# Performance work log

Measured on AMD Instinct MI355X. Metric: run time of the kernel, lower is better.

The kernel has to match this reference:

```python
import jax, jax.numpy as jnp
import numpy as np

N, L, C, K = 8, 16384, 256, 64  # batch, points, d_color, anchor_num; d_struct = 4*K = 256


def setup_inputs() -> dict:
    key = jax.random.key(0)
    ks = jax.random.split(key, 12)
    d_in = C + 4 * K  # 512
    s1, s2, s3 = 1.0 / np.sqrt(d_in), 1.0 / np.sqrt(128), 1.0 / np.sqrt(256)
    return {
        'feat0': jax.random.normal(ks[0], (N, L, C), jnp.float32),
        'feat1': jax.random.normal(ks[1], (N, L, C), jnp.float32),
        'pts_3d0': jax.random.normal(ks[2], (N, L, 3), jnp.float32),
        'pts_3d1': jax.random.normal(ks[3], (N, L, 3), jnp.float32),
        'anchor_i': jax.random.randint(ks[4], (N, K), 0, L, jnp.int32),
        'anchor_j': jax.random.randint(ks[5], (N, K), 0, L, jnp.int32),
        'W1': jax.random.uniform(ks[6], (d_in, 128), jnp.float32, -s1, s1),
        'b1': jax.random.uniform(ks[7], (128,), jnp.float32, -s1, s1),
        'W2': jax.random.uniform(ks[8], (128, 256), jnp.float32, -s2, s2),
        'b2': jax.random.uniform(ks[9], (256,), jnp.float32, -s2, s2),
        'W3': jax.random.uniform(ks[10], (256, C), jnp.float32, -s3, s3),
        'b3': jax.random.uniform(ks[11], (C,), jnp.float32, -s3, s3),
    }


def _structured(pts, anchor_idx):
    # pts: [N,L,3], anchor_idx: [N,K] -> [N,L,4K]
    anchors = jnp.take_along_axis(pts, anchor_idx[:, :, None], axis=1)  # [N,K,3]
    diff = pts[:, :, None, :] - anchors[:, None, :, :]                  # [N,L,K,3]
    dist = jnp.sum(diff * diff, axis=-1, keepdims=True)                 # [N,L,K,1]
    f = jnp.concatenate([diff, dist], axis=-1)                          # [N,L,K,4]
    f = f / jnp.sum(jnp.abs(f), axis=-2, keepdims=True)                 # L1 norm over K
    f = jnp.swapaxes(f, -1, -2).reshape(pts.shape[0], pts.shape[1], -1)  # [N,L,4K]
    # original l1_norm is @torch.no_grad -> structured feature is detached
    return jax.lax.stop_gradient(f)


def _mlp(x, W1, b1, W2, b2, W3, b3):
    h = jax.nn.relu(x @ W1 + b1)
    h = jax.nn.relu(h @ W2 + b2)  # dropout is identity in eval
    return h @ W3 + b3


def reference(feat0, feat1, pts_3d0, pts_3d1, anchor_i, anchor_j,
              W1, b1, W2, b2, W3, b3):
    s0 = _structured(pts_3d0, anchor_i)
    s1 = _structured(pts_3d1, anchor_j)
    aug0 = _mlp(jnp.concatenate([feat0, s0], axis=-1), W1, b1, W2, b2, W3, b3)
    aug1 = _mlp(jnp.concatenate([feat1, s1], axis=-1), W1, b1, W2, b2, W3, b3)
    return aug0, aug1
```

## Files before the change

kernel.cpp:

```cpp
#include <hip/hip_runtime.h>

typedef __bf16 bf16x8 __attribute__((ext_vector_type(8)));
typedef float f32x4 __attribute__((ext_vector_type(4)));
typedef unsigned short u16x4 __attribute__((ext_vector_type(4)));
typedef unsigned short u16x8 __attribute__((ext_vector_type(8)));

#define NBATCH 8
#define LPTS   16384
#define CDIM   256
#define KANC   64
#define DIN    512
#define H1DIM  128
#define H2DIM  256
#define TM     64

__device__ __forceinline__ unsigned short f2b(float f){
  __bf16 h = (__bf16)f;
  return __builtin_bit_cast(unsigned short, h);
}

__global__ __launch_bounds__(256) void prep_weights(
    const float* __restrict__ W1, const float* __restrict__ W2,
    const float* __restrict__ W3, unsigned short* __restrict__ wt){
  int id = blockIdx.x * 256 + threadIdx.x;
  if (id < 65536){
    int r = id >> 9, c = id & 511;
    wt[id] = f2b(W1[c * 128 + r]);
  } else if (id < 98304){
    int t = id - 65536; int r = t >> 7, c = t & 127;
    wt[id] = f2b(W2[c * 256 + r]);
  } else if (id < 163840){
    int t = id - 98304; int r = t >> 8, c = t & 255;
    wt[id] = f2b(W3[c * 256 + r]);
  }
}

__global__ __launch_bounds__(512, 4) void fused(
    const float* __restrict__ feat0, const float* __restrict__ feat1,
    const float* __restrict__ pts0, const float* __restrict__ pts1,
    const int* __restrict__ anc_i, const int* __restrict__ anc_j,
    const float* __restrict__ b1, const float* __restrict__ b2,
    const float* __restrict__ b3, const unsigned short* __restrict__ wt,
    float* __restrict__ out)
{
  __shared__ unsigned short xs[TM * DIN];
  __shared__ unsigned short h1s[TM * H1DIM];
  unsigned short* h2s = xs;
  float4* anc4 = (float4*)h1s;

  const int tid  = threadIdx.x;
  const int wg   = blockIdx.x;
  const int strm = wg >> 11;
  const int n    = (wg >> 8) & 7;
  const int l0   = (wg & 255) * TM;

  const float* feat = strm ? feat1 : feat0;
  const float* pts  = strm ? pts1 : pts0;
  const int*   anci = strm ? anc_j : anc_i;

  const float* pp = pts + ((size_t)n * LPTS + l0 + (tid >> 3)) * 3;
  float px = pp[0], py = pp[1], pz = pp[2];

  if (tid < KANC){
    int ai = anci[n * KANC + tid];
    const float* ap = pts + ((size_t)n * LPTS + ai) * 3;
    anc4[tid + (tid >> 3)] = make_float4(ap[0], ap[1], ap[2], 0.f);
  }

  {
    const float4* fb = (const float4*)(feat + ((size_t)n * LPTS + l0) * CDIM);
    #pragma unroll
    for (int it = 0; it < 8; ++it){
      int flat = it * 512 + tid;
      int r = flat >> 6, c4 = flat & 63;
      float4 v = fb[flat];
      int e = (r * DIN + c4 * 4) ^ ((r & 7) << 3);
      u16x4 pk = { f2b(v.x), f2b(v.y), f2b(v.z), f2b(v.w) };
      *(u16x4*)&xs[e] = pk;
    }
  }
  __syncthreads();

  {
    const int l   = tid >> 3;
    const int sub = tid & 7;
    float s0 = 0.f, s1 = 0.f, s2 = 0.f, s3 = 0.f;
    #pragma unroll
    for (int i = 0; i < 8; ++i){
      float4 a = anc4[sub * 9 + i];
      float dx = px - a.x, dy = py - a.y, dz = pz - a.z;
      float d2 = dx*dx + dy*dy + dz*dz;
      s0 += fabsf(dx); s1 += fabsf(dy); s2 += fabsf(dz); s3 += d2;
    }
    #pragma unroll
    for (int m = 1; m <= 4; m <<= 1){
      s0 += __shfl_xor(s0, m, 64);
      s1 += __shfl_xor(s1, m, 64);
      s2 += __shfl_xor(s2, m, 64);
      s3 += __shfl_xor(s3, m, 64);
    }
    float i0 = 1.f/s0, i1 = 1.f/s1, i2 = 1.f/s2, i3 = 1.f/s3;

    u16x8 o0, o1, o2, o3;
    #pragma unroll
    for (int i = 0; i < 8; ++i){
      float4 a = anc4[sub * 9 + i];
      float dx = px - a.x, dy = py - a.y, dz = pz - a.z;
      float d2 = dx*dx + dy*dy + dz*dz;
      o0[i] = f2b(dx * i0); o1[i] = f2b(dy * i1);
      o2[i] = f2b(dz * i2); o3[i] = f2b(d2 * i3);
    }
    int base = l * DIN + 256 + sub * 8;
    int swl = (l & 7) << 3;
    *(u16x8*)&xs[(base      ) ^ swl] = o0;
    *(u16x8*)&xs[(base +  64) ^ swl] = o1;
    *(u16x8*)&xs[(base + 128) ^ swl] = o2;
    *(u16x8*)&xs[(base + 192) ^ swl] = o3;
  }
  __syncthreads();

  const int lane = tid & 63;
  const int w    = tid >> 6;
  const int lr   = lane & 15;
  const int lg   = lane >> 4;

  {
    f32x4 acc[4] = {};
    const int col = w * 16 + lr;
    const unsigned short* wrow = wt + col * DIN;
    #pragma unroll 4
    for (int kk = 0; kk < 16; ++kk){
      int kb = kk * 32 + lg * 8;
      bf16x8 b = *(const bf16x8*)&wrow[kb];
      #pragma unroll
      for (int m = 0; m < 4; ++m){
        int row = m * 16 + lr;
        int e = (row * DIN + kb) ^ ((row & 7) << 3);
        bf16x8 a = *(const bf16x8*)&xs[e];
        acc[m] = __builtin_amdgcn_mfma_f32_16x16x32_bf16(a, b, acc[m], 0, 0, 0);
      }
    }
    float bias = b1[col];
    #pragma unroll
    for (int m = 0; m < 4; ++m){
      #pragma unroll
      for (int r = 0; r < 4; ++r){
        int row = m * 16 + lg * 4 + r;
        float v = fmaxf(acc[m][r] + bias, 0.f);
        int e = (row * H1DIM + col) ^ ((row & 7) << 3);
        h1s[e] = f2b(v);
      }
    }
  }
  __syncthreads();

  {
    const unsigned short* w2t = wt + 65536;
    f32x4 acc[4][2] = {};
    const int col0 = w * 32;
    #pragma unroll
    for (int kk = 0; kk < 4; ++kk){
      int kb = kk * 32 + lg * 8;
      bf16x8 bf0 = *(const bf16x8*)&w2t[(col0 + lr) * H1DIM + kb];
      bf16x8 bf1 = *(const bf16x8*)&w2t[(col0 + 16 + lr) * H1DIM + kb];
      #pragma unroll
      for (int m = 0; m < 4; ++m){
        int row = m * 16 + lr;
        int e = (row * H1DIM + kb) ^ ((row & 7) << 3);
        bf16x8 a = *(const bf16x8*)&h1s[e];
        acc[m][0] = __builtin_amdgcn_mfma_f32_16x16x32_bf16(a, bf0, acc[m][0], 0, 0, 0);
        acc[m][1] = __builtin_amdgcn_mfma_f32_16x16x32_bf16(a, bf1, acc[m][1], 0, 0, 0);
      }
    }
    __syncthreads();
    #pragma unroll
    for (int nt = 0; nt < 2; ++nt){
      int col = col0 + nt * 16 + lr;
      float bias = b2[col];
      #pragma unroll
      for (int m = 0; m < 4; ++m){
        #pragma unroll
        for (int r = 0; r < 4; ++r){
          int row = m * 16 + lg * 4 + r;
          float v = fmaxf(acc[m][nt][r] + bias, 0.f);
          int e = (row * H2DIM + col) ^ ((row & 7) << 3);
          h2s[e] = f2b(v);
        }
      }
    }
  }
  __syncthreads();

  {
    const unsigned short* w3t = wt + 98304;
    f32x4 acc[4][2] = {};
    const int col0 = w * 32;
    #pragma unroll 4
    for (int kk = 0; kk < 8; ++kk){
      int kb = kk * 32 + lg * 8;
      bf16x8 bf0 = *(const bf16x8*)&w3t[(col0 + lr) * H2DIM + kb];
      bf16x8 bf1 = *(const bf16x8*)&w3t[(col0 + 16 + lr) * H2DIM + kb];
      #pragma unroll
      for (int m = 0; m < 4; ++m){
        int row = m * 16 + lr;
        int e = (row * H2DIM + kb) ^ ((row & 7) << 3);
        bf16x8 a = *(const bf16x8*)&h2s[e];
        acc[m][0] = __builtin_amdgcn_mfma_f32_16x16x32_bf16(a, bf0, acc[m][0], 0, 0, 0);
        acc[m][1] = __builtin_amdgcn_mfma_f32_16x16x32_bf16(a, bf1, acc[m][1], 0, 0, 0);
      }
    }
    float* ob = out + (((size_t)strm * NBATCH + n) * LPTS + l0) * CDIM;
    #pragma unroll
    for (int nt = 0; nt < 2; ++nt){
      int col = col0 + nt * 16 + lr;
      float bias = b3[col];
      #pragma unroll
      for (int m = 0; m < 4; ++m){
        #pragma unroll
        for (int r = 0; r < 4; ++r){
          int row = m * 16 + lg * 4 + r;
          ob[(size_t)row * CDIM + col] = acc[m][nt][r] + bias;
        }
      }
    }
  }
}

extern "C" void kernel_launch(void* const* d_in, const int* in_sizes, int n_in,
                              void* d_out, int out_size, void* d_ws, size_t ws_size,
                              hipStream_t stream){
  const float* feat0 = (const float*)d_in[0];
  const float* feat1 = (const float*)d_in[1];
  const float* pts0  = (const float*)d_in[2];
  const float* pts1  = (const float*)d_in[3];
  const int*   anci  = (const int*)d_in[4];
  const int*   ancj  = (const int*)d_in[5];
  const float* W1    = (const float*)d_in[6];
  const float* b1    = (const float*)d_in[7];
  const float* W2    = (const float*)d_in[8];
  const float* b2    = (const float*)d_in[9];
  const float* W3    = (const float*)d_in[10];
  const float* b3    = (const float*)d_in[11];
  unsigned short* wt = (unsigned short*)d_ws;
  float* out = (float*)d_out;

  prep_weights<<<640, 256, 0, stream>>>(W1, W2, W3, wt);
  fused<<<4096, 512, 0, stream>>>(feat0, feat1, pts0, pts1, anci, ancj,
                                  b1, b2, b3, wt, out);
}
```

Measured before the change: 226.9 us.

## Make fused MLP kernel persistent over 8 tiles with register-prefetched inputs

Each workgroup now handles 8 consecutive 64-row tiles instead of one, cutting the grid from 4096 to 512 blocks. The feature and point loads for the next tile are issued into registers while the current tile's structured features and GEMMs run, overlapping global reads with compute. Bias values are hoisted out of the loop, and barriers become a custom lgkmcnt-wait plus s_barrier that does not wait on outstanding global loads. The costs are higher register pressure from the prefetch buffer, fewer blocks to fill the GPU (512 for 256 CUs), and the anchor table being reloaded into shared memory every iteration.

```diff
diff --git a/kernel.cpp b/kernel.cpp
--- a/kernel.cpp
+++ b/kernel.cpp
@@ -18,6 +18,12 @@
   __bf16 h = (__bf16)f;
   return __builtin_bit_cast(unsigned short, h);
 }
+
+#define LBAR() do{ \
+  asm volatile("s_waitcnt lgkmcnt(0)" ::: "memory"); \
+  __builtin_amdgcn_s_barrier(); \
+  asm volatile("" ::: "memory"); \
+} while(0)
 
 __global__ __launch_bounds__(256) void prep_weights(
     const float* __restrict__ W1, const float* __restrict__ W2,
@@ -49,180 +55,202 @@
   float4* anc4 = (float4*)h1s;
 
   const int tid  = threadIdx.x;
-  const int wg   = blockIdx.x;
-  const int strm = wg >> 11;
-  const int n    = (wg >> 8) & 7;
-  const int l0   = (wg & 255) * TM;
+  const int b    = blockIdx.x;
+  const int strm = b >> 8;
+  const int n    = (b >> 5) & 7;
+  const int tb   = b & 31;
 
   const float* feat = strm ? feat1 : feat0;
   const float* pts  = strm ? pts1 : pts0;
   const int*   anci = strm ? anc_j : anc_i;
 
-  const float* pp = pts + ((size_t)n * LPTS + l0 + (tid >> 3)) * 3;
-  float px = pp[0], py = pp[1], pz = pp[2];
+  const int lane = tid & 63;
+  const int w    = tid >> 6;
+  const int lr   = lane & 15, lg = lane >> 4;
+
+  const int col1 = w * 16 + lr;
+  const unsigned short* wrow1 = wt + col1 * DIN;
+  const float bias1v = b1[col1];
+  const int col23 = w * 32;
+  const float bias2v0 = b2[col23 + lr], bias2v1 = b2[col23 + 16 + lr];
+  const float bias3v0 = b3[col23 + lr], bias3v1 = b3[col23 + 16 + lr];
+  const unsigned short* w2t = wt + 65536;
+  const unsigned short* w3t = wt + 98304;
+
+  const size_t fB = (size_t)n * LPTS;
 
   if (tid < KANC){
     int ai = anci[n * KANC + tid];
-    const float* ap = pts + ((size_t)n * LPTS + ai) * 3;
+    const float* ap = pts + (fB + ai) * 3;
     anc4[tid + (tid >> 3)] = make_float4(ap[0], ap[1], ap[2], 0.f);
   }
 
+  float4 fv[8];
   {
-    const float4* fb = (const float4*)(feat + ((size_t)n * LPTS + l0) * CDIM);
+    const float4* fb = (const float4*)(feat + (fB + tb * 512) * CDIM);
+    #pragma unroll
+    for (int it = 0; it < 8; ++it) fv[it] = fb[it * 512 + tid];
+  }
+  float px, py, pz;
+  {
+    const float* pp = pts + (fB + tb * 512 + (tid >> 3)) * 3;
+    px = pp[0]; py = pp[1]; pz = pp[2];
+  }
+  __syncthreads();
+
+  #pragma unroll 1
+  for (int i = 0; i < 8; ++i){
+    const int l0i = tb * 512 + i * 64;
+
     #pragma unroll
     for (int it = 0; it < 8; ++it){
       int flat = it * 512 + tid;
       int r = flat >> 6, c4 = flat & 63;
-      float4 v = fb[flat];
+      float4 v = fv[it];
       int e = (r * DIN + c4 * 4) ^ ((r & 7) << 3);
       u16x4 pk = { f2b(v.x), f2b(v.y), f2b(v.z), f2b(v.w) };
       *(u16x4*)&xs[e] = pk;
     }
-  }
-  __syncthreads();
-
-  {
-    const int l   = tid >> 3;
-    const int sub = tid & 7;
-    float s0 = 0.f, s1 = 0.f, s2 = 0.f, s3 = 0.f;
-    #pragma unroll
-    for (int i = 0; i < 8; ++i){
-      float4 a = anc4[sub * 9 + i];
-      float dx = px - a.x, dy = py - a.y, dz = pz - a.z;
-      float d2 = dx*dx + dy*dy + dz*dz;
-      s0 += fabsf(dx); s1 += fabsf(dy); s2 += fabsf(dz); s3 += d2;
-    }
-    #pragma unroll
-    for (int m = 1; m <= 4; m <<= 1){
-      s0 += __shfl_xor(s0, m, 64);
-      s1 += __shfl_xor(s1, m, 64);
-      s2 += __shfl_xor(s2, m, 64);
-      s3 += __shfl_xor(s3, m, 64);
-    }
-    float i0 = 1.f/s0, i1 = 1.f/s1, i2 = 1.f/s2, i3 = 1.f/s3;
-
-    u16x8 o0, o1, o2, o3;
-    #pragma unroll
-    for (int i = 0; i < 8; ++i){
-      float4 a = anc4[sub * 9 + i];
-      float dx = px - a.x, dy = py - a.y, dz = pz - a.z;
-      float d2 = dx*dx + dy*dy + dz*dz;
-      o0[i] = f2b(dx * i0); o1[i] = f2b(dy * i1);
-      o2[i] = f2b(dz * i2); o3[i] = f2b(d2 * i3);
-    }
-    int base = l * DIN + 256 + sub * 8;
-    int swl = (l & 7) << 3;
-    *(u16x8*)&xs[(base      ) ^ swl] = o0;
-    *(u16x8*)&xs[(base +  64) ^ swl] = o1;
-    *(u16x8*)&xs[(base + 128) ^ swl] = o2;
-    *(u16x8*)&xs[(base + 192) ^ swl] = o3;
-  }
-  __syncthreads();
-
-  const int lane = tid & 63;
-  const int w    = tid >> 6;
-  const int lr   = lane & 15;
-  const int lg   = lane >> 4;
-
-  {
-    f32x4 acc[4] = {};
-    const int col = w * 16 + lr;
-    const unsigned short* wrow = wt + col * DIN;
-    #pragma unroll 4
-    for (int kk = 0; kk < 16; ++kk){
-      int kb = kk * 32 + lg * 8;
-      bf16x8 b = *(const bf16x8*)&wrow[kb];
-      #pragma unroll
-      for (int m = 0; m < 4; ++m){
-        int row = m * 16 + lr;
-        int e = (row * DIN + kb) ^ ((row & 7) << 3);
-        bf16x8 a = *(const bf16x8*)&xs[e];
-        acc[m] = __builtin_amdgcn_mfma_f32_16x16x32_bf16(a, b, acc[m], 0, 0, 0);
-      }
-    }
-    float bias = b1[col];
-    #pragma unroll
-    for (int m = 0; m < 4; ++m){
-      #pragma unroll
-      for (int r = 0; r < 4; ++r){
-        int row = m * 16 + lg * 4 + r;
-        float v = fmaxf(acc[m][r] + bias, 0.f);
-        int e = (row * H1DIM + col) ^ ((row & 7) << 3);
-        h1s[e] = f2b(v);
-      }
-    }
-  }
-  __syncthreads();
-
-  {
-    const unsigned short* w2t = wt + 65536;
-    f32x4 acc[4][2] = {};
-    const int col0 = w * 32;
-    #pragma unroll
-    for (int kk = 0; kk < 4; ++kk){
-      int kb = kk * 32 + lg * 8;
-      bf16x8 bf0 = *(const bf16x8*)&w2t[(col0 + lr) * H1DIM + kb];
-      bf16x8 bf1 = *(const bf16x8*)&w2t[(col0 + 16 + lr) * H1DIM + kb];
-      #pragma unroll
-      for (int m = 0; m < 4; ++m){
-        int row = m * 16 + lr;
-        int e = (row * H1DIM + kb) ^ ((row & 7) << 3);
-        bf16x8 a = *(const bf16x8*)&h1s[e];
-        acc[m][0] = __builtin_amdgcn_mfma_f32_16x16x32_bf16(a, bf0, acc[m][0], 0, 0, 0);
-        acc[m][1] = __builtin_amdgcn_mfma_f32_16x16x32_bf16(a, bf1, acc[m][1], 0, 0, 0);
-      }
-    }
-    __syncthreads();
-    #pragma unroll
-    for (int nt = 0; nt < 2; ++nt){
-      int col = col0 + nt * 16 + lr;
-      float bias = b2[col];
+
+    {
+      const int l = tid >> 3, sub = tid & 7;
+      float s0 = 0.f, s1 = 0.f, s2 = 0.f, s3 = 0.f;
+      #pragma unroll
+      for (int k = 0; k < 8; ++k){
+        float4 a = anc4[sub * 9 + k];
+        float dx = px - a.x, dy = py - a.y, dz = pz - a.z;
+        float d2 = dx*dx + dy*dy + dz*dz;
+        s0 += fabsf(dx); s1 += fabsf(dy); s2 += fabsf(dz); s3 += d2;
+      }
+      #pragma unroll
+      for (int m = 1; m <= 4; m <<= 1){
+        s0 += __shfl_xor(s0, m, 64);
+        s1 += __shfl_xor(s1, m, 64);
+        s2 += __shfl_xor(s2, m, 64);
+        s3 += __shfl_xor(s3, m, 64);
+      }
+      float i0 = 1.f/s0, i1 = 1.f/s1, i2 = 1.f/s2, i3 = 1.f/s3;
+
+      u16x8 o0, o1, o2, o3;
+      #pragma unroll
+      for (int k = 0; k < 8; ++k){
+        float4 a = anc4[sub * 9 + k];
+        float dx = px - a.x, dy = py - a.y, dz = pz - a.z;
+        float d2 = dx*dx + dy*dy + dz*dz;
+        o0[k] = f2b(dx * i0); o1[k] = f2b(dy * i1);
+        o2[k] = f2b(dz * i2); o3[k] = f2b(d2 * i3);
+      }
+      int base = l * DIN + 256 + sub * 8;
+      int swl = (l & 7) << 3;
+      *(u16x8*)&xs[(base      ) ^ swl] = o0;
+      *(u16x8*)&xs[(base +  64) ^ swl] = o1;
+      *(u16x8*)&xs[(base + 128) ^ swl] = o2;
+      *(u16x8*)&xs[(base + 192) ^ swl] = o3;
+    }
+
+    if (i < 7){
+      const float4* fbn = (const float4*)(feat + (fB + l0i + 64) * CDIM);
+      #pragma unroll
+      for (int it = 0; it < 8; ++it) fv[it] = fbn[it * 512 + tid];
+      const float* ppn = pts + (fB + l0i + 64 + (tid >> 3)) * 3;
+      px = ppn[0]; py = ppn[1]; pz = ppn[2];
+    }
+    LBAR();
+
+    {
+      f32x4 acc[4] = {};
+      #pragma unroll 4
+      for (int kk = 0; kk < 16; ++kk){
+        int kb = kk * 32 + lg * 8;
+        bf16x8 bfr = *(const bf16x8*)&wrow1[kb];
+        #pragma unroll
+        for (int m = 0; m < 4; ++m){
+          int row = m * 16 + lr;
+          bf16x8 a = *(const bf16x8*)&xs[(row * DIN + kb) ^ ((row & 7) << 3)];
+          acc[m] = __builtin_amdgcn_mfma_f32_16x16x32_bf16(a, bfr, acc[m], 0, 0, 0);
+        }
+      }
       #pragma unroll
       for (int m = 0; m < 4; ++m){
         #pragma unroll
         for (int r = 0; r < 4; ++r){
           int row = m * 16 + lg * 4 + r;
-          float v = fmaxf(acc[m][nt][r] + bias, 0.f);
-          int e = (row * H2DIM + col) ^ ((row & 7) << 3);
-          h2s[e] = f2b(v);
-        }
-      }
-    }
-  }
-  __syncthreads();
-
-  {
-    const unsigned short* w3t = wt + 98304;
-    f32x4 acc[4][2] = {};
-    const int col0 = w * 32;
-    #pragma unroll 4
-    for (int kk = 0; kk < 8; ++kk){
-      int kb = kk * 32 + lg * 8;
-      bf16x8 bf0 = *(const bf16x8*)&w3t[(col0 + lr) * H2DIM + kb];
-      bf16x8 bf1 = *(const bf16x8*)&w3t[(col0 + 16 + lr) * H2DIM + kb];
-      #pragma unroll
-      for (int m = 0; m < 4; ++m){
-        int row = m * 16 + lr;
-        int e = (row * H2DIM + kb) ^ ((row & 7) << 3);
-        bf16x8 a = *(const bf16x8*)&h2s[e];
-        acc[m][0] = __builtin_amdgcn_mfma_f32_16x16x32_bf16(a, bf0, acc[m][0], 0, 0, 0);
-        acc[m][1] = __builtin_amdgcn_mfma_f32_16x16x32_bf16(a, bf1, acc[m][1], 0, 0, 0);
-      }
-    }
-    float* ob = out + (((size_t)strm * NBATCH + n) * LPTS + l0) * CDIM;
-    #pragma unroll
-    for (int nt = 0; nt < 2; ++nt){
-      int col = col0 + nt * 16 + lr;
-      float bias = b3[col];
-      #pragma unroll
-      for (int m = 0; m < 4; ++m){
-        #pragma unroll
-        for (int r = 0; r < 4; ++r){
-          int row = m * 16 + lg * 4 + r;
-          ob[(size_t)row * CDIM + col] = acc[m][nt][r] + bias;
-        }
-      }
-    }
+          float v = fmaxf(acc[m][r] + bias1v, 0.f);
+          h1s[(row * H1DIM + col1) ^ ((row & 7) << 3)] = f2b(v);
+        }
+      }
+    }
+    LBAR();
+
+    {
+      f32x4 acc[4][2] = {};
+      #pragma unroll
+      for (int kk = 0; kk < 4; ++kk){
+        int kb = kk * 32 + lg * 8;
+        bf16x8 bf0 = *(const bf16x8*)&w2t[(col23 + lr) * H1DIM + kb];
+        bf16x8 bf1 = *(const bf16x8*)&w2t[(col23 + 16 + lr) * H1DIM + kb];
+        #pragma unroll
+        for (int m = 0; m < 4; ++m){
+          int row = m * 16 + lr;
+          bf16x8 a = *(const bf16x8*)&h1s[(row * H1DIM + kb) ^ ((row & 7) << 3)];
+          acc[m][0] = __builtin_amdgcn_mfma_f32_16x16x32_bf16(a, bf0, acc[m][0], 0, 0, 0);
+          acc[m][1] = __builtin_amdgcn_mfma_f32_16x16x32_bf16(a, bf1, acc[m][1], 0, 0, 0);
+        }
+      }
+      LBAR();
+      #pragma unroll
+      for (int nt = 0; nt < 2; ++nt){
+        float bias = nt ? bias2v1 : bias2v0;
+        int col = col23 + nt * 16 + lr;
+        #pragma unroll
+        for (int m = 0; m < 4; ++m){
+          #pragma unroll
+          for (int r = 0; r < 4; ++r){
+            int row = m * 16 + lg * 4 + r;
+            float v = fmaxf(acc[m][nt][r] + bias, 0.f);
+            h2s[(row * H2DIM + col) ^ ((row & 7) << 3)] = f2b(v);
+          }
+        }
+      }
+    }
+    LBAR();
+
+    {
+      if (i < 7 && tid < KANC){
+        int ai = anci[n * KANC + tid];
+        const float* ap = pts + (fB + ai) * 3;
+        anc4[tid + (tid >> 3)] = make_float4(ap[0], ap[1], ap[2], 0.f);
+      }
+      f32x4 acc[4][2] = {};
+      #pragma unroll 4
+      for (int kk = 0; kk < 8; ++kk){
+        int kb = kk * 32 + lg * 8;
+        bf16x8 bf0 = *(const bf16x8*)&w3t[(col23 + lr) * H2DIM + kb];
+        bf16x8 bf1 = *(const bf16x8*)&w3t[(col23 + 16 + lr) * H2DIM + kb];
+        #pragma unroll
+        for (int m = 0; m < 4; ++m){
+          int row = m * 16 + lr;
+          bf16x8 a = *(const bf16x8*)&h2s[(row * H2DIM + kb) ^ ((row & 7) << 3)];
+          acc[m][0] = __builtin_amdgcn_mfma_f32_16x16x32_bf16(a, bf0, acc[m][0], 0, 0, 0);
+          acc[m][1] = __builtin_amdgcn_mfma_f32_16x16x32_bf16(a, bf1, acc[m][1], 0, 0, 0);
+        }
+      }
+      float* ob = out + (((size_t)strm * NBATCH + n) * LPTS + l0i) * CDIM;
+      #pragma unroll
+      for (int nt = 0; nt < 2; ++nt){
+        float bias = nt ? bias3v1 : bias3v0;
+        int col = col23 + nt * 16 + lr;
+        #pragma unroll
+        for (int m = 0; m < 4; ++m){
+          #pragma unroll
+          for (int r = 0; r < 4; ++r){
+            int row = m * 16 + lg * 4 + r;
+            ob[(size_t)row * CDIM + col] = acc[m][nt][r] + bias;
+          }
+        }
+      }
+    }
+    LBAR();
   }
 }
 
@@ -245,6 +273,6 @@
   float* out = (float*)d_out;
 
   prep_weights<<<640, 256, 0, stream>>>(W1, W2, W3, wt);
-  fused<<<4096, 512, 0, stream>>>(feat0, feat1, pts0, pts1, anci, ancj,
-                                  b1, b2, b3, wt, out);
-}
+  fused<<<512, 512, 0, stream>>>(feat0, feat1, pts0, pts1, anci, ancj,
+                                 b1, b2, b3, wt, out);
+}
```

Result: slower. 517.4 us (+128.0%).

## Stream feat directly into layer-1 MFMA operands and shrink LDS tile

Applied to the files above, without the earlier changes.

Layer 1 no longer stages the color features in shared memory. Each wave now loads fp32 feat rows from global memory, converts them to bf16 in registers and feeds them straight to MFMA, while LDS holds only the structured half of the input. Layer 1 is re-tiled into a 2x4 wave grid with 32x32 output blocks. The smaller LDS footprint lets the launch bounds ask for 6 blocks per CU instead of 4, and a barrier in layer 2 that is now redundant is removed. The cost is that the four column-waves sharing a row block each re-read the same feat rows, relying on cache hits, and global load latency now sits directly in the MFMA loop.

```diff
diff --git a/kernel.cpp b/kernel.cpp
--- a/kernel.cpp
+++ b/kernel.cpp
@@ -2,7 +2,6 @@
 
 typedef __bf16 bf16x8 __attribute__((ext_vector_type(8)));
 typedef float f32x4 __attribute__((ext_vector_type(4)));
-typedef unsigned short u16x4 __attribute__((ext_vector_type(4)));
 typedef unsigned short u16x8 __attribute__((ext_vector_type(8)));
 
 #define NBATCH 8
@@ -17,6 +16,13 @@
 __device__ __forceinline__ unsigned short f2b(float f){
   __bf16 h = (__bf16)f;
   return __builtin_bit_cast(unsigned short, h);
+}
+
+__device__ __forceinline__ bf16x8 cvt8(float4 a, float4 b){
+  bf16x8 r;
+  r[0]=(__bf16)a.x; r[1]=(__bf16)a.y; r[2]=(__bf16)a.z; r[3]=(__bf16)a.w;
+  r[4]=(__bf16)b.x; r[5]=(__bf16)b.y; r[6]=(__bf16)b.z; r[7]=(__bf16)b.w;
+  return r;
 }
 
 __global__ __launch_bounds__(256) void prep_weights(
@@ -35,7 +41,7 @@
   }
 }
 
-__global__ __launch_bounds__(512, 4) void fused(
+__global__ __launch_bounds__(512, 6) void fused(
     const float* __restrict__ feat0, const float* __restrict__ feat1,
     const float* __restrict__ pts0, const float* __restrict__ pts1,
     const int* __restrict__ anc_i, const int* __restrict__ anc_j,
@@ -43,7 +49,7 @@
     const float* __restrict__ b3, const unsigned short* __restrict__ wt,
     float* __restrict__ out)
 {
-  __shared__ unsigned short xs[TM * DIN];
+  __shared__ unsigned short xs[TM * 256];
   __shared__ unsigned short h1s[TM * H1DIM];
   unsigned short* h2s = xs;
   float4* anc4 = (float4*)h1s;
@@ -58,26 +64,15 @@
   const float* pts  = strm ? pts1 : pts0;
   const int*   anci = strm ? anc_j : anc_i;
 
-  const float* pp = pts + ((size_t)n * LPTS + l0 + (tid >> 3)) * 3;
+  const size_t fB = (size_t)n * LPTS;
+
+  const float* pp = pts + (fB + l0 + (tid >> 3)) * 3;
   float px = pp[0], py = pp[1], pz = pp[2];
 
   if (tid < KANC){
     int ai = anci[n * KANC + tid];
-    const float* ap = pts + ((size_t)n * LPTS + ai) * 3;
+    const float* ap = pts + (fB + ai) * 3;
     anc4[tid + (tid >> 3)] = make_float4(ap[0], ap[1], ap[2], 0.f);
-  }
-
-  {
-    const float4* fb = (const float4*)(feat + ((size_t)n * LPTS + l0) * CDIM);
-    #pragma unroll
-    for (int it = 0; it < 8; ++it){
-      int flat = it * 512 + tid;
-      int r = flat >> 6, c4 = flat & 63;
-      float4 v = fb[flat];
-      int e = (r * DIN + c4 * 4) ^ ((r & 7) << 3);
-      u16x4 pk = { f2b(v.x), f2b(v.y), f2b(v.z), f2b(v.w) };
-      *(u16x4*)&xs[e] = pk;
-    }
   }
   __syncthreads();
 
@@ -110,7 +105,7 @@
       o0[i] = f2b(dx * i0); o1[i] = f2b(dy * i1);
       o2[i] = f2b(dz * i2); o3[i] = f2b(d2 * i3);
     }
-    int base = l * DIN + 256 + sub * 8;
+    int base = l * 256 + sub * 8;
     int swl = (l & 7) << 3;
     *(u16x8*)&xs[(base      ) ^ swl] = o0;
     *(u16x8*)&xs[(base +  64) ^ swl] = o1;
@@ -121,34 +116,54 @@
 
   const int lane = tid & 63;
   const int w    = tid >> 6;
-  const int lr   = lane & 15;
-  const int lg   = lane >> 4;
-
-  {
-    f32x4 acc[4] = {};
-    const int col = w * 16 + lr;
-    const unsigned short* wrow = wt + col * DIN;
-    #pragma unroll 4
-    for (int kk = 0; kk < 16; ++kk){
-      int kb = kk * 32 + lg * 8;
-      bf16x8 b = *(const bf16x8*)&wrow[kb];
-      #pragma unroll
-      for (int m = 0; m < 4; ++m){
-        int row = m * 16 + lr;
-        int e = (row * DIN + kb) ^ ((row & 7) << 3);
-        bf16x8 a = *(const bf16x8*)&xs[e];
-        acc[m] = __builtin_amdgcn_mfma_f32_16x16x32_bf16(a, b, acc[m], 0, 0, 0);
-      }
-    }
-    float bias = b1[col];
-    #pragma unroll
-    for (int m = 0; m < 4; ++m){
-      #pragma unroll
-      for (int r = 0; r < 4; ++r){
-        int row = m * 16 + lg * 4 + r;
-        float v = fmaxf(acc[m][r] + bias, 0.f);
-        int e = (row * H1DIM + col) ^ ((row & 7) << 3);
-        h1s[e] = f2b(v);
+  const int lr   = lane & 15, lg = lane >> 4;
+
+  {
+    const int wr = w >> 2, wc = w & 3;
+    f32x4 acc[2][2] = {};
+    const float* f0 = feat + (fB + l0 + wr * 32 + lr) * (size_t)CDIM;
+    const float* f1 = f0 + 16 * (size_t)CDIM;
+    const unsigned short* bq0 = wt + (wc * 32      + lr) * DIN;
+    const unsigned short* bq1 = wt + (wc * 32 + 16 + lr) * DIN;
+
+    #pragma unroll
+    for (int kk = 0; kk < 8; ++kk){
+      int kf = kk * 32 + lg * 8;
+      bf16x8 b0  = *(const bf16x8*)&bq0[kf];
+      bf16x8 b1v = *(const bf16x8*)&bq1[kf];
+      float4 lo0 = *(const float4*)&f0[kf], hi0 = *(const float4*)&f0[kf + 4];
+      float4 lo1 = *(const float4*)&f1[kf], hi1 = *(const float4*)&f1[kf + 4];
+      bf16x8 a0 = cvt8(lo0, hi0), a1 = cvt8(lo1, hi1);
+      acc[0][0] = __builtin_amdgcn_mfma_f32_16x16x32_bf16(a0, b0,  acc[0][0], 0, 0, 0);
+      acc[0][1] = __builtin_amdgcn_mfma_f32_16x16x32_bf16(a0, b1v, acc[0][1], 0, 0, 0);
+      acc[1][0] = __builtin_amdgcn_mfma_f32_16x16x32_bf16(a1, b0,  acc[1][0], 0, 0, 0);
+      acc[1][1] = __builtin_amdgcn_mfma_f32_16x16x32_bf16(a1, b1v, acc[1][1], 0, 0, 0);
+    }
+    const int row0 = wr * 32 + lr, row1 = row0 + 16;
+    #pragma unroll
+    for (int kk = 0; kk < 8; ++kk){
+      int ks = kk * 32 + lg * 8;
+      bf16x8 b0  = *(const bf16x8*)&bq0[256 + ks];
+      bf16x8 b1v = *(const bf16x8*)&bq1[256 + ks];
+      bf16x8 a0 = *(const bf16x8*)&xs[(row0 * 256 + ks) ^ ((row0 & 7) << 3)];
+      bf16x8 a1 = *(const bf16x8*)&xs[(row1 * 256 + ks) ^ ((row1 & 7) << 3)];
+      acc[0][0] = __builtin_amdgcn_mfma_f32_16x16x32_bf16(a0, b0,  acc[0][0], 0, 0, 0);
+      acc[0][1] = __builtin_amdgcn_mfma_f32_16x16x32_bf16(a0, b1v, acc[0][1], 0, 0, 0);
+      acc[1][0] = __builtin_amdgcn_mfma_f32_16x16x32_bf16(a1, b0,  acc[1][0], 0, 0, 0);
+      acc[1][1] = __builtin_amdgcn_mfma_f32_16x16x32_bf16(a1, b1v, acc[1][1], 0, 0, 0);
+    }
+    #pragma unroll
+    for (int nn = 0; nn < 2; ++nn){
+      int col = wc * 32 + nn * 16 + lr;
+      float bias = b1[col];
+      #pragma unroll
+      for (int m = 0; m < 2; ++m){
+        #pragma unroll
+        for (int r = 0; r < 4; ++r){
+          int row = wr * 32 + m * 16 + lg * 4 + r;
+          float v = fmaxf(acc[m][nn][r] + bias, 0.f);
+          h1s[(row * H1DIM + col) ^ ((row & 7) << 3)] = f2b(v);
+        }
       }
     }
   }
@@ -166,13 +181,11 @@
       #pragma unroll
       for (int m = 0; m < 4; ++m){
         int row = m * 16 + lr;
-        int e = (row * H1DIM + kb) ^ ((row & 7) << 3);
-        bf16x8 a = *(const bf16x8*)&h1s[e];
+        bf16x8 a = *(const bf16x8*)&h1s[(row * H1DIM + kb) ^ ((row & 7) << 3)];
         acc[m][0] = __builtin_amdgcn_mfma_f32_16x16x32_bf16(a, bf0, acc[m][0], 0, 0, 0);
         acc[m][1] = __builtin_amdgcn_mfma_f32_16x16x32_bf16(a, bf1, acc[m][1], 0, 0, 0);
       }
     }
-    __syncthreads();
     #pragma unroll
     for (int nt = 0; nt < 2; ++nt){
       int col = col0 + nt * 16 + lr;
@@ -183,8 +196,7 @@
         for (int r = 0; r < 4; ++r){
           int row = m * 16 + lg * 4 + r;
           float v = fmaxf(acc[m][nt][r] + bias, 0.f);
-          int e = (row * H2DIM + col) ^ ((row & 7) << 3);
-          h2s[e] = f2b(v);
+          h2s[(row * H2DIM + col) ^ ((row & 7) << 3)] = f2b(v);
         }
       }
     }
@@ -203,8 +215,7 @@
       #pragma unroll
       for (int m = 0; m < 4; ++m){
         int row = m * 16 + lr;
-        int e = (row * H2DIM + kb) ^ ((row & 7) << 3);
-        bf16x8 a = *(const bf16x8*)&h2s[e];
+        bf16x8 a = *(const bf16x8*)&h2s[(row * H2DIM + kb) ^ ((row & 7) << 3)];
         acc[m][0] = __builtin_amdgcn_mfma_f32_16x16x32_bf16(a, bf0, acc[m][0], 0, 0, 0);
         acc[m][1] = __builtin_amdgcn_mfma_f32_16x16x32_bf16(a, bf1, acc[m][1], 0, 0, 0);
       }
```

New measurement: 379.7 us. 67.3% more time.

## Fold structured-feature GEMM into per-batch coefficients, halving layer-1 K dimension

Applied to the files above, without the earlier changes.

The structured anchor features are linear in a few per-point scalars (p, |p|^2 and the L1 normalisers), so their contribution to layer 1 is rewritten as 11 per-column coefficients precomputed per (stream, batch) in a small prep kernel. The fused kernel now stages only the 256 colour channels in LDS, runs half the layer-1 MFMA iterations, and adds the structured term in the epilogue from per-row scalars. Less LDS also allows a higher occupancy hint, and one barrier in layer 2 is removed. The structured term is now computed in fp32 rather than through bf16 inputs, which changes rounding, and the squared-distance sum is expanded algebraically, which risks cancellation.

```diff
diff --git a/kernel.cpp b/kernel.cpp
--- a/kernel.cpp
+++ b/kernel.cpp
@@ -3,7 +3,6 @@
 typedef __bf16 bf16x8 __attribute__((ext_vector_type(8)));
 typedef float f32x4 __attribute__((ext_vector_type(4)));
 typedef unsigned short u16x4 __attribute__((ext_vector_type(4)));
-typedef unsigned short u16x8 __attribute__((ext_vector_type(8)));
 
 #define NBATCH 8
 #define LPTS   16384
@@ -35,16 +34,59 @@
   }
 }
 
-__global__ __launch_bounds__(512, 4) void fused(
+__global__ __launch_bounds__(128) void prep_coef(
+    const float* __restrict__ pts0, const float* __restrict__ pts1,
+    const int* __restrict__ anc_i, const int* __restrict__ anc_j,
+    const float* __restrict__ W1, float* __restrict__ coef){
+  const int comb = blockIdx.x;
+  const int strm = comb >> 3, n = comb & 7;
+  const int col  = threadIdx.x;
+  __shared__ float4 anc[64];
+  const float* pts  = strm ? pts1 : pts0;
+  const int*   anci = strm ? anc_j : anc_i;
+  if (col < 64){
+    int ai = anci[n * KANC + col];
+    const float* ap = pts + ((size_t)n * LPTS + ai) * 3;
+    anc[col] = make_float4(ap[0], ap[1], ap[2], 0.f);
+  }
+  __syncthreads();
+  float SX=0,CX=0,SY=0,CY=0,SZ=0,CZ=0,SD=0,ADx=0,ADy=0,ADz=0,CD2=0;
+  float SAx=0,SAy=0,SAz=0,SA2=0;
+  for (int k = 0; k < KANC; ++k){
+    float4 a = anc[k];
+    float ak2 = a.x*a.x + a.y*a.y + a.z*a.z;
+    float wx = W1[(256 + k) * 128 + col];
+    float wy = W1[(320 + k) * 128 + col];
+    float wz = W1[(384 + k) * 128 + col];
+    float wd = W1[(448 + k) * 128 + col];
+    SX += wx; CX += a.x * wx;
+    SY += wy; CY += a.y * wy;
+    SZ += wz; CZ += a.z * wz;
+    SD += wd; ADx += a.x * wd; ADy += a.y * wd; ADz += a.z * wd;
+    CD2 += ak2 * wd;
+    SAx += a.x; SAy += a.y; SAz += a.z; SA2 += ak2;
+  }
+  float* cf = coef + (size_t)comb * 12 * 128;
+  cf[ 0*128+col]=SX;  cf[ 1*128+col]=CX;  cf[ 2*128+col]=SY;  cf[ 3*128+col]=CY;
+  cf[ 4*128+col]=SZ;  cf[ 5*128+col]=CZ;  cf[ 6*128+col]=SD;  cf[ 7*128+col]=ADx;
+  cf[ 8*128+col]=ADy; cf[ 9*128+col]=ADz; cf[10*128+col]=CD2;
+  if (col == 0) cf[11*128+0] = SAx;
+  if (col == 1) cf[11*128+1] = SAy;
+  if (col == 2) cf[11*128+2] = SAz;
+  if (col == 3) cf[11*128+3] = SA2;
+}
+
+__global__ __launch_bounds__(512, 6) void fused(
     const float* __restrict__ feat0, const float* __restrict__ feat1,
     const float* __restrict__ pts0, const float* __restrict__ pts1,
     const int* __restrict__ anc_i, const int* __restrict__ anc_j,
     const float* __restrict__ b1, const float* __restrict__ b2,
     const float* __restrict__ b3, const unsigned short* __restrict__ wt,
-    float* __restrict__ out)
+    const float* __restrict__ coef, float* __restrict__ out)
 {
-  __shared__ unsigned short xs[TM * DIN];
+  __shared__ unsigned short xs[TM * 256];
   __shared__ unsigned short h1s[TM * H1DIM];
+  __shared__ float scal[TM][12];
   unsigned short* h2s = xs;
   float4* anc4 = (float4*)h1s;
 
@@ -57,9 +99,11 @@
   const float* feat = strm ? feat1 : feat0;
   const float* pts  = strm ? pts1 : pts0;
   const int*   anci = strm ? anc_j : anc_i;
+  const float* cf   = coef + (size_t)((strm << 3) | n) * 12 * 128;
 
   const float* pp = pts + ((size_t)n * LPTS + l0 + (tid >> 3)) * 3;
   float px = pp[0], py = pp[1], pz = pp[2];
+  float SAx = cf[11*128+0], SAy = cf[11*128+1], SAz = cf[11*128+2], SA2 = cf[11*128+3];
 
   if (tid < KANC){
     int ai = anci[n * KANC + tid];
@@ -74,7 +118,7 @@
       int flat = it * 512 + tid;
       int r = flat >> 6, c4 = flat & 63;
       float4 v = fb[flat];
-      int e = (r * DIN + c4 * 4) ^ ((r & 7) << 3);
+      int e = (r * 256 + c4 * 4) ^ ((r & 7) << 3);
       u16x4 pk = { f2b(v.x), f2b(v.y), f2b(v.z), f2b(v.w) };
       *(u16x4*)&xs[e] = pk;
     }
@@ -84,38 +128,37 @@
   {
     const int l   = tid >> 3;
     const int sub = tid & 7;
-    float s0 = 0.f, s1 = 0.f, s2 = 0.f, s3 = 0.f;
+    float s0 = 0.f, s1 = 0.f, s2 = 0.f;
     #pragma unroll
     for (int i = 0; i < 8; ++i){
       float4 a = anc4[sub * 9 + i];
-      float dx = px - a.x, dy = py - a.y, dz = pz - a.z;
-      float d2 = dx*dx + dy*dy + dz*dz;
-      s0 += fabsf(dx); s1 += fabsf(dy); s2 += fabsf(dz); s3 += d2;
+      s0 += fabsf(px - a.x); s1 += fabsf(py - a.y); s2 += fabsf(pz - a.z);
     }
     #pragma unroll
     for (int m = 1; m <= 4; m <<= 1){
       s0 += __shfl_xor(s0, m, 64);
       s1 += __shfl_xor(s1, m, 64);
       s2 += __shfl_xor(s2, m, 64);
-      s3 += __shfl_xor(s3, m, 64);
-    }
+    }
+    float pp2 = px*px + py*py + pz*pz;
+    float s3 = 64.f * pp2 - 2.f * (px*SAx + py*SAy + pz*SAz) + SA2;
     float i0 = 1.f/s0, i1 = 1.f/s1, i2 = 1.f/s2, i3 = 1.f/s3;
-
-    u16x8 o0, o1, o2, o3;
-    #pragma unroll
-    for (int i = 0; i < 8; ++i){
-      float4 a = anc4[sub * 9 + i];
-      float dx = px - a.x, dy = py - a.y, dz = pz - a.z;
-      float d2 = dx*dx + dy*dy + dz*dz;
-      o0[i] = f2b(dx * i0); o1[i] = f2b(dy * i1);
-      o2[i] = f2b(dz * i2); o3[i] = f2b(d2 * i3);
-    }
-    int base = l * DIN + 256 + sub * 8;
-    int swl = (l & 7) << 3;
-    *(u16x8*)&xs[(base      ) ^ swl] = o0;
-    *(u16x8*)&xs[(base +  64) ^ swl] = o1;
-    *(u16x8*)&xs[(base + 128) ^ swl] = o2;
-    *(u16x8*)&xs[(base + 192) ^ swl] = o3;
+    float u;
+    switch (sub){
+      case 0: u = i0 * px;       break;
+      case 1: u = -i0;           break;
+      case 2: u = i1 * py;       break;
+      case 3: u = -i1;           break;
+      case 4: u = i2 * pz;       break;
+      case 5: u = -i2;           break;
+      case 6: u = i3 * pp2;      break;
+      default: u = -2.f*i3*px;   break;
+    }
+    scal[l][sub] = u;
+    if (sub < 3){
+      float u2 = (sub == 0) ? -2.f*i3*py : (sub == 1) ? -2.f*i3*pz : i3;
+      scal[l][8 + sub] = u2;
+    }
   }
   __syncthreads();
 
@@ -128,15 +171,17 @@
     f32x4 acc[4] = {};
     const int col = w * 16 + lr;
     const unsigned short* wrow = wt + col * DIN;
+    float cc[11];
+    #pragma unroll
+    for (int j = 0; j < 11; ++j) cc[j] = cf[j * 128 + col];
     #pragma unroll 4
-    for (int kk = 0; kk < 16; ++kk){
+    for (int kk = 0; kk < 8; ++kk){
       int kb = kk * 32 + lg * 8;
       bf16x8 b = *(const bf16x8*)&wrow[kb];
       #pragma unroll
       for (int m = 0; m < 4; ++m){
         int row = m * 16 + lr;
-        int e = (row * DIN + kb) ^ ((row & 7) << 3);
-        bf16x8 a = *(const bf16x8*)&xs[e];
+        bf16x8 a = *(const bf16x8*)&xs[(row * 256 + kb) ^ ((row & 7) << 3)];
         acc[m] = __builtin_amdgcn_mfma_f32_16x16x32_bf16(a, b, acc[m], 0, 0, 0);
       }
     }
@@ -146,9 +191,15 @@
       #pragma unroll
       for (int r = 0; r < 4; ++r){
         int row = m * 16 + lg * 4 + r;
-        float v = fmaxf(acc[m][r] + bias, 0.f);
-        int e = (row * H1DIM + col) ^ ((row & 7) << 3);
-        h1s[e] = f2b(v);
+        f32x4 ua = *(const f32x4*)&scal[row][0];
+        f32x4 ub = *(const f32x4*)&scal[row][4];
+        f32x4 uc = *(const f32x4*)&scal[row][8];
+        float s = acc[m][r] + bias;
+        s += ua[0]*cc[0] + ua[1]*cc[1] + ua[2]*cc[2] + ua[3]*cc[3];
+        s += ub[0]*cc[4] + ub[1]*cc[5] + ub[2]*cc[6] + ub[3]*cc[7];
+        s += uc[0]*cc[8] + uc[1]*cc[9] + uc[2]*cc[10];
+        float v = fmaxf(s, 0.f);
+        h1s[(row * H1DIM + col) ^ ((row & 7) << 3)] = f2b(v);
       }
     }
   }
@@ -166,13 +217,11 @@
       #pragma unroll
       for (int m = 0; m < 4; ++m){
         int row = m * 16 + lr;
-        int e = (row * H1DIM + kb) ^ ((row & 7) << 3);
-        bf16x8 a = *(const bf16x8*)&h1s[e];
+        bf16x8 a = *(const bf16x8*)&h1s[(row * H1DIM + kb) ^ ((row & 7) << 3)];
         acc[m][0] = __builtin_amdgcn_mfma_f32_16x16x32_bf16(a, bf0, acc[m][0], 0, 0, 0);
         acc[m][1] = __builtin_amdgcn_mfma_f32_16x16x32_bf16(a, bf1, acc[m][1], 0, 0, 0);
       }
     }
-    __syncthreads();
     #pragma unroll
     for (int nt = 0; nt < 2; ++nt){
       int col = col0 + nt * 16 + lr;
@@ -183,8 +232,7 @@
         for (int r = 0; r < 4; ++r){
           int row = m * 16 + lg * 4 + r;
           float v = fmaxf(acc[m][nt][r] + bias, 0.f);
-          int e = (row * H2DIM + col) ^ ((row & 7) << 3);
-          h2s[e] = f2b(v);
+          h2s[(row * H2DIM + col) ^ ((row & 7) << 3)] = f2b(v);
         }
       }
     }
@@ -203,8 +251,7 @@
       #pragma unroll
       for (int m = 0; m < 4; ++m){
         int row = m * 16 + lr;
-        int e = (row * H2DIM + kb) ^ ((row & 7) << 3);
-        bf16x8 a = *(const bf16x8*)&h2s[e];
+        bf16x8 a = *(const bf16x8*)&h2s[(row * H2DIM + kb) ^ ((row & 7) << 3)];
         acc[m][0] = __builtin_amdgcn_mfma_f32_16x16x32_bf16(a, bf0, acc[m][0], 0, 0, 0);
         acc[m][1] = __builtin_amdgcn_mfma_f32_16x16x32_bf16(a, bf1, acc[m][1], 0, 0, 0);
       }
@@ -242,9 +289,11 @@
   const float* W3    = (const float*)d_in[10];
   const float* b3    = (const float*)d_in[11];
   unsigned short* wt = (unsigned short*)d_ws;
+  float* coef = (float*)((char*)d_ws + 163840 * sizeof(unsigned short));
   float* out = (float*)d_out;
 
   prep_weights<<<640, 256, 0, stream>>>(W1, W2, W3, wt);
+  prep_coef<<<16, 128, 0, stream>>>(pts0, pts1, anci, ancj, W1, coef);
   fused<<<4096, 512, 0, stream>>>(feat0, feat1, pts0, pts1, anci, ancj,
-                                  b1, b2, b3, wt, out);
-}
+                                  b1, b2, b3, wt, coef, out);
+}
```

New measurement: 234.6 us. 1.03x slower.
